# Optimization experiments

Measured on AMD Instinct MI355X. Metric: run time of the kernel, lower is better.

## Reference

```python
import jax, jax.numpy as jnp
import numpy as np

N = 100000  # nodes
E = 1600000  # directed edges

_DIMS = [("eg1", 3, 160), ("eg2", 160, 80), ("eg3", 80, 40), ("eg4", 40, 20),
         ("el1", 20, 10), ("el2", 10, 3), ("dl1", 3, 10), ("dl2", 10, 20),
         ("dg1", 20, 40), ("dg2", 40, 80), ("dg3", 80, 160), ("dg4", 160, 3)]


def _lin_init(key, ci, co):
    s = 1.0 / np.sqrt(ci)
    kw, kb = jax.random.split(key)
    w = jax.random.uniform(kw, (ci, co), jnp.float32, -s, s)
    b = jax.random.uniform(kb, (co,), jnp.float32, -s, s)
    return w, b


def setup_inputs():
    key = jax.random.key(0)
    k0, k1, k2 = jax.random.split(key, 3)
    x = jax.random.normal(k0, (N, 3), jnp.float32)
    src = jax.random.randint(k1, (E,), 0, N)
    dst = jax.random.randint(k2, (E,), 0, N)
    edge_index = jnp.stack([src, dst])  # [2, E] int32 indices
    out = {"x": x, "edge_index": edge_index}
    for i, (name, ci, co) in enumerate(_DIMS):
        w, b = _lin_init(jax.random.fold_in(key, i + 10), ci, co)
        out[name + "_w"] = w
        out[name + "_b"] = b
    return out


def _gcn(x, w, b, src, dst, norm):
    # PyG GCNConv: linear transform, then symmetric-normalized scatter-add.
    h = x @ w
    agg = jax.ops.segment_sum(h[src] * norm[:, None], dst, num_segments=N)
    return agg + b


def reference(x, edge_index, eg1_w, eg1_b, eg2_w, eg2_b, eg3_w, eg3_b, eg4_w, eg4_b,
              el1_w, el1_b, el2_w, el2_b, dl1_w, dl1_b, dl2_w, dl2_b,
              dg1_w, dg1_b, dg2_w, dg2_b, dg3_w, dg3_b, dg4_w, dg4_b):
    loops = jnp.arange(N)
    src = jnp.concatenate([edge_index[0], loops])  # add self-loops (PyG default)
    dst = jnp.concatenate([edge_index[1], loops])
    deg = jax.ops.segment_sum(jnp.ones(src.shape[0], x.dtype), dst, num_segments=N)
    dis = jnp.where(deg > 0, jax.lax.rsqrt(deg), 0.0)
    norm = dis[src] * dis[dst]  # D^-1/2 A D^-1/2 edge weights
    relu = jax.nn.relu
    h = relu(_gcn(x, eg1_w, eg1_b, src, dst, norm))
    h = relu(_gcn(h, eg2_w, eg2_b, src, dst, norm))
    h = relu(_gcn(h, eg3_w, eg3_b, src, dst, norm))
    h = relu(_gcn(h, eg4_w, eg4_b, src, dst, norm))
    h = relu(h @ el1_w + el1_b)
    h = h @ el2_w + el2_b  # latent [N, 3]
    h = relu(h @ dl1_w + dl1_b)
    h = relu(h @ dl2_w + dl2_b)
    h = relu(_gcn(h, dg1_w, dg1_b, src, dst, norm))
    h = relu(_gcn(h, dg2_w, dg2_b, src, dst, norm))
    h = relu(_gcn(h, dg3_w, dg3_b, src, dst, norm))
    h = jnp.tanh(_gcn(h, dg4_w, dg4_b, src, dst, norm))
    return h
```

## Files before the change

### kernel.cpp

```cpp
#include <hip/hip_runtime.h>
#include <hip/hip_fp16.h>
#include <math.h>

#define BS 256
static constexpr int NN = 100000;
static constexpr int EE = 1600000;
static constexpr int BUCKET_SH = 7;
static constexpr int NBUCKET = (NN + 127) >> BUCKET_SH;
static constexpr int NB_PART = 256;
static constexpr int CHUNK = EE / NB_PART;
static constexpr int NP = NBUCKET * NB_PART;
static constexpr int SCAN_ELEMS = 1024;
static constexpr int NPB = (NP + SCAN_ELEMS - 1) / SCAN_ELEMS;

static inline int cdiv(long long a, int b) { return (int)((a + b - 1) / b); }

template <int ACT>
__device__ __forceinline__ float act_f(float v) {
    if (ACT == 1) return fmaxf(v, 0.0f);
    if (ACT == 2) return tanhf(v);
    return v;
}

__device__ __forceinline__ unsigned short h16(float v) {
    return __half_as_ushort(__float2half(v));
}
__device__ __forceinline__ unsigned pack2h(float a, float b) {
    return (unsigned)h16(a) | ((unsigned)h16(b) << 16);
}
__device__ __forceinline__ float4 cvt4h(uint2 r) {
    float2 fa = __half22float2(*(const __half2*)&r.x);
    float2 fb = __half22float2(*(const __half2*)&r.y);
    return make_float4(fa.x, fa.y, fb.x, fb.y);
}

template <int OUTM>
__device__ __forceinline__ void store1(float* out, size_t idx, float v, float dn) {
    if (OUTM == 0) out[idx] = v;
    else if (OUTM == 1) out[idx] = v * dn;
    else if (OUTM == 2) ((unsigned short*)out)[idx] = h16(v * dn);
    else ((unsigned short*)out)[idx] = h16(v);
}

__global__ __launch_bounds__(256) void k_hist(const int* __restrict__ dst,
                                              int* __restrict__ part_cnt) {
    __shared__ int h[NBUCKET];
    int b = blockIdx.x;
    for (int j = threadIdx.x; j < NBUCKET; j += 256) h[j] = 0;
    __syncthreads();
    int e0 = b * CHUNK;
    for (int k = threadIdx.x; k < CHUNK; k += 256)
        atomicAdd(&h[dst[e0 + k] >> BUCKET_SH], 1);
    __syncthreads();
    for (int j = threadIdx.x; j < NBUCKET; j += 256)
        part_cnt[j * NB_PART + b] = h[j];
}

__global__ void k_scanA(const int* __restrict__ in, int* __restrict__ outp,
                        int* __restrict__ bsums) {
    __shared__ int lds[BS];
    int base = blockIdx.x * SCAN_ELEMS;
    int t = threadIdx.x;
    int v[4];
    int s = 0;
#pragma unroll
    for (int j = 0; j < 4; ++j) {
        int idx = base + t * 4 + j;
        v[j] = (idx < NP) ? in[idx] : 0;
        s += v[j];
    }
    lds[t] = s;
    __syncthreads();
    for (int off = 1; off < BS; off <<= 1) {
        int add = (t >= off) ? lds[t - off] : 0;
        __syncthreads();
        lds[t] += add;
        __syncthreads();
    }
    int run = lds[t] - s;
    if (t == BS - 1) bsums[blockIdx.x] = lds[BS - 1];
#pragma unroll
    for (int j = 0; j < 4; ++j) {
        int idx = base + t * 4 + j;
        if (idx < NP) outp[idx] = run;
        run += v[j];
    }
}

__global__ void k_scanB(int* __restrict__ bsums) {
    if (threadIdx.x == 0 && blockIdx.x == 0) {
        int acc = 0;
        for (int i = 0; i < NPB; ++i) {
            int t = bsums[i];
            bsums[i] = acc;
            acc += t;
        }
    }
}

__global__ void k_scanC(int* __restrict__ outp, const int* __restrict__ bsums,
                        int* __restrict__ bbase) {
    int i = blockIdx.x * BS + threadIdx.x;
    if (i < NP) {
        int v = outp[i] + bsums[i / SCAN_ELEMS];
        outp[i] = v;
        if ((i & (NB_PART - 1)) == 0) bbase[i / NB_PART] = v;
    }
    if (i == 0) bbase[NBUCKET] = EE;
}

__global__ __launch_bounds__(256) void k_part(const int* __restrict__ src,
                                              const int* __restrict__ dst,
                                              const int* __restrict__ scan_out,
                                              unsigned* __restrict__ epb) {
    __shared__ int cur[NBUCKET];
    int b = blockIdx.x;
    for (int j = threadIdx.x; j < NBUCKET; j += 256) cur[j] = scan_out[j * NB_PART + b];
    __syncthreads();
    int e0 = b * CHUNK;
    for (int k = threadIdx.x; k < CHUNK; k += 256) {
        int e = e0 + k;
        int d = dst[e];
        int s = src[e];
        int pos = atomicAdd(&cur[d >> BUCKET_SH], 1);
        epb[pos] = ((unsigned)(d & ((1 << BUCKET_SH) - 1)) << 17) | (unsigned)s;
    }
}

__global__ __launch_bounds__(256) void k_fine2(const int* __restrict__ bbase,
                                               const unsigned* __restrict__ epb,
                                               int* __restrict__ eidx,
                                               int* __restrict__ rowptr,
                                               float* __restrict__ dis) {
    __shared__ int hcnt[1 << BUCKET_SH];
    __shared__ int hoff[1 << BUCKET_SH];
    int b = blockIdx.x;
    int n0 = b << BUCKET_SH;
    int nloc = min(1 << BUCKET_SH, NN - n0);
    int t = threadIdx.x;
    if (t < (1 << BUCKET_SH)) hcnt[t] = 0;
    __syncthreads();
    int es = bbase[b], ee = bbase[b + 1];
    for (int k = es + t; k < ee; k += 256) atomicAdd(&hcnt[epb[k] >> 17], 1);
    __syncthreads();
    if (t < (1 << BUCKET_SH)) hoff[t] = hcnt[t];
    __syncthreads();
    for (int off = 1; off < (1 << BUCKET_SH); off <<= 1) {
        int add = (t >= off && t < (1 << BUCKET_SH)) ? hoff[t - off] : 0;
        __syncthreads();
        if (t < (1 << BUCKET_SH)) hoff[t] += add;
        __syncthreads();
    }
    if (t < nloc) {
        int excl = hoff[t] - hcnt[t];
        rowptr[n0 + t] = es + excl;
        dis[n0 + t] = rsqrtf((float)(hcnt[t] + 1));
    }
    __syncthreads();
    if (t < (1 << BUCKET_SH)) hoff[t] = es + hoff[t] - hcnt[t];
    __syncthreads();
    for (int k = es + t; k < ee; k += 256) {
        unsigned p = epb[k];
        int pos = atomicAdd(&hoff[p >> 17], 1);
        eidx[pos] = (int)(p & 0x1FFFFu);
    }
    if (b == NBUCKET - 1 && t == 0) rowptr[NN] = EE;
}

template <int C, int ACT, bool HASB>
__global__ void k_gatherh(const unsigned short* __restrict__ g, const int* __restrict__ rowptr,
                          const int* __restrict__ eidx, const float* __restrict__ dis,
                          const float* __restrict__ b, float* __restrict__ out) {
    static_assert(C % 4 == 0, "C%4");
    constexpr int V = C / 4;
    int t = blockIdx.x * BS + threadIdx.x;
    if (t >= NN * V) return;
    int n = t / V, v = t % V;
    const uint2* g2 = (const uint2*)g;
    float4 acc = cvt4h(g2[(size_t)n * V + v]);
    int rs = rowptr[n], re = rowptr[n + 1];
    int k = rs;
    for (; k + 4 <= re; k += 4) {
        int s0 = eidx[k + 0], s1 = eidx[k + 1], s2 = eidx[k + 2], s3 = eidx[k + 3];
        uint2 r0 = g2[(size_t)s0 * V + v];
        uint2 r1 = g2[(size_t)s1 * V + v];
        uint2 r2 = g2[(size_t)s2 * V + v];
        uint2 r3 = g2[(size_t)s3 * V + v];
        float4 h0 = cvt4h(r0), h1 = cvt4h(r1), h2 = cvt4h(r2), h3 = cvt4h(r3);
        acc.x += (h0.x + h1.x) + (h2.x + h3.x);
        acc.y += (h0.y + h1.y) + (h2.y + h3.y);
        acc.z += (h0.z + h1.z) + (h2.z + h3.z);
        acc.w += (h0.w + h1.w) + (h2.w + h3.w);
    }
    for (; k < re; ++k) {
        float4 hv = cvt4h(g2[(size_t)eidx[k] * V + v]);
        acc.x += hv.x; acc.y += hv.y; acc.z += hv.z; acc.w += hv.w;
    }
    float dn = dis[n];
    acc.x *= dn; acc.y *= dn; acc.z *= dn; acc.w *= dn;
    if (HASB) {
        float4 bb = ((const float4*)b)[v];
        acc.x += bb.x; acc.y += bb.y; acc.z += bb.z; acc.w += bb.w;
    }
    acc.x = act_f<ACT>(acc.x);
    acc.y = act_f<ACT>(acc.y);
    acc.z = act_f<ACT>(acc.z);
    acc.w = act_f<ACT>(acc.w);
    ((float4*)out)[(size_t)n * V + v] = acc;
}

template <int ACT, bool HASB>
__global__ void k_gather3d(const float* __restrict__ g, const int* __restrict__ rowptr,
                           const int* __restrict__ eidx, const float* __restrict__ dis,
                           const float* __restrict__ b, float* __restrict__ out) {
    int n = blockIdx.x * BS + threadIdx.x;
    if (n >= NN) return;
    const float* gp = g + (size_t)n * 3;
    float a0 = gp[0], a1 = gp[1], a2 = gp[2];
    int rs = rowptr[n], re = rowptr[n + 1];
    int k = rs;
    for (; k + 4 <= re; k += 4) {
        const float* q0 = g + (size_t)eidx[k + 0] * 3;
        const float* q1 = g + (size_t)eidx[k + 1] * 3;
        const float* q2 = g + (size_t)eidx[k + 2] * 3;
        const float* q3 = g + (size_t)eidx[k + 3] * 3;
        float b00 = q0[0], b01 = q0[1], b02 = q0[2];
        float b10 = q1[0], b11 = q1[1], b12 = q1[2];
        float b20 = q2[0], b21 = q2[1], b22 = q2[2];
        float b30 = q3[0], b31 = q3[1], b32 = q3[2];
        a0 += (b00 + b10) + (b20 + b30);
        a1 += (b01 + b11) + (b21 + b31);
        a2 += (b02 + b12) + (b22 + b32);
    }
    for (; k < re; ++k) {
        const float* gq = g + (size_t)eidx[k] * 3;
        a0 += gq[0]; a1 += gq[1]; a2 += gq[2];
    }
    float dn = dis[n];
    a0 *= dn; a1 *= dn; a2 *= dn;
    if (HASB) { a0 += b[0]; a1 += b[1]; a2 += b[2]; }
    float* op = out + (size_t)n * 3;
    op[0] = act_f<ACT>(a0);
    op[1] = act_f<ACT>(a1);
    op[2] = act_f<ACT>(a2);
}

__global__ void k_scale3(const float* __restrict__ x, const float* __restrict__ dis,
                         float* __restrict__ g) {
    int i = blockIdx.x * BS + threadIdx.x;
    if (i < NN * 3) g[i] = x[i] * dis[i / 3];
}

template <int CIN, int COUT, int TC, int TN, int TM, int BK, int ACT, bool HASB, int OUTM, bool INH>
__global__ __launch_bounds__(256) void k_mm_tiled(const float* __restrict__ x,
                                                  const float* __restrict__ w,
                                                  const float* __restrict__ b,
                                                  float* __restrict__ out,
                                                  const float* __restrict__ dis) {
    constexpr int TR = 256 / TC;
    constexpr int BM = TR * TM;
    constexpr int LDA = BM + 4;
    constexpr int CHUNKS = CIN / BK;
    constexpr int BK4 = BK / 4;
    constexpr int CIN4 = CIN / 4;
    static_assert(TC * TN == COUT, "cols");
    static_assert(CIN % BK == 0 && BK % 4 == 0, "bk");
    static_assert(TM == 4 || TM == 8, "tm");
    __shared__ float As[BK * LDA];
    __shared__ float Ws[BK * COUT];
    const int tid = threadIdx.x;
    const int tc = tid % TC, tr = tid / TC;
    const int n0 = blockIdx.x * BM;

    float acc[TM][TN];
#pragma unroll
    for (int r = 0; r < TM; ++r)
#pragma unroll
        for (int j = 0; j < TN; ++j) acc[r][j] = HASB ? b[tc * TN + j] : 0.0f;

    const float4* x4 = (const float4*)x;
    const uint2* xh = (const uint2*)x;
    const float4* w4 = (const float4*)w;

    for (int ch = 0; ch < CHUNKS; ++ch) {
        const int kb4 = ch * BK4;
        if (ch) __syncthreads();
        for (int i = tid; i < BM * BK4; i += 256) {
            int r = i / BK4, k4 = i % BK4;
            int row = n0 + r;
            float4 v = make_float4(0.f, 0.f, 0.f, 0.f);
            if (row < NN) {
                if (INH) v = cvt4h(xh[(size_t)row * CIN4 + kb4 + k4]);
                else v = x4[(size_t)row * CIN4 + kb4 + k4];
            }
            int base = (4 * k4) * LDA + r;
            As[base] = v.x;
            As[base + LDA] = v.y;
            As[base + 2 * LDA] = v.z;
            As[base + 3 * LDA] = v.w;
        }
        for (int i = tid; i < BK * COUT / 4; i += 256) {
            ((float4*)Ws)[i] = w4[(size_t)kb4 * COUT + i];
        }
        __syncthreads();
#pragma unroll 4
        for (int k = 0; k < BK; ++k) {
            float a[TM];
            *(float4*)&a[0] = *(const float4*)&As[k * LDA + tr * TM];
            if (TM == 8) *(float4*)&a[4] = *(const float4*)&As[k * LDA + tr * TM + 4];
            float wr[TN];
#pragma unroll
            for (int j = 0; j < TN; ++j) wr[j] = Ws[k * COUT + tc * TN + j];
#pragma unroll
            for (int r = 0; r < TM; ++r)
#pragma unroll
                for (int j = 0; j < TN; ++j) acc[r][j] = fmaf(a[r], wr[j], acc[r][j]);
        }
    }
#pragma unroll
    for (int r = 0; r < TM; ++r) {
        int row = n0 + tr * TM + r;
        if (row < NN) {
            float dn = (OUTM == 1 || OUTM == 2) ? dis[row] : 0.0f;
            size_t base = (size_t)row * COUT + tc * TN;
#pragma unroll
            for (int j = 0; j < TN; ++j) store1<OUTM>(out, base + j, act_f<ACT>(acc[r][j]), dn);
        }
    }
}

template <int CIN, int COUT, int ACT, bool HASB, int OUTM>
__global__ void k_mm_vec4(const float* __restrict__ x, const float* __restrict__ w,
                          const float* __restrict__ b, float* __restrict__ out,
                          const float* __restrict__ dis) {
    static_assert(CIN % 4 == 0 && COUT % 4 == 0, "align");
    constexpr int TM = 8;
    constexpr int CIN4 = CIN / 4;
    constexpr int COUT4 = COUT / 4;
    constexpr int RG = NN / TM;
    int i = blockIdx.x * BS + threadIdx.x;
    if (i >= RG * COUT4) return;
    int c4 = i % COUT4;
    int n0 = (i / COUT4) * TM;
    const float4* x4 = (const float4*)x;
    const float4* w4 = (const float4*)w;
    float4 acc[TM];
    float4 bb = HASB ? ((const float4*)b)[c4] : make_float4(0.f, 0.f, 0.f, 0.f);
#pragma unroll
    for (int r = 0; r < TM; ++r) acc[r] = bb;
    for (int k4 = 0; k4 < CIN4; ++k4) {
        float4 wv[4];
#pragma unroll
        for (int j = 0; j < 4; ++j) wv[j] = w4[(size_t)(4 * k4 + j) * COUT4 + c4];
#pragma unroll
        for (int r = 0; r < TM; ++r) {
            float4 xv = x4[(size_t)(n0 + r) * CIN4 + k4];
            acc[r].x = fmaf(xv.x, wv[0].x, fmaf(xv.y, wv[1].x, fmaf(xv.z, wv[2].x, fmaf(xv.w, wv[3].x, acc[r].x))));
            acc[r].y = fmaf(xv.x, wv[0].y, fmaf(xv.y, wv[1].y, fmaf(xv.z, wv[2].y, fmaf(xv.w, wv[3].y, acc[r].y))));
            acc[r].z = fmaf(xv.x, wv[0].z, fmaf(xv.y, wv[1].z, fmaf(xv.z, wv[2].z, fmaf(xv.w, wv[3].z, acc[r].z))));
            acc[r].w = fmaf(xv.x, wv[0].w, fmaf(xv.y, wv[1].w, fmaf(xv.z, wv[2].w, fmaf(xv.w, wv[3].w, acc[r].w))));
        }
    }
#pragma unroll
    for (int r = 0; r < TM; ++r) {
        float vx = act_f<ACT>(acc[r].x), vy = act_f<ACT>(acc[r].y);
        float vz = act_f<ACT>(acc[r].z), vw = act_f<ACT>(acc[r].w);
        size_t gi = (size_t)(n0 + r) * COUT4 + c4;
        if (OUTM == 2) {
            float dn = dis[n0 + r];
            uint2 u;
            u.x = pack2h(vx * dn, vy * dn);
            u.y = pack2h(vz * dn, vw * dn);
            ((uint2*)out)[gi] = u;
        } else if (OUTM == 1) {
            float dn = dis[n0 + r];
            ((float4*)out)[gi] = make_float4(vx * dn, vy * dn, vz * dn, vw * dn);
        } else {
            ((float4*)out)[gi] = make_float4(vx, vy, vz, vw);
        }
    }
}

template <int CIN, int COUT, int ACT, int OUTM>
__global__ void k_mm_rowbcast(const float* __restrict__ x, const float* __restrict__ w,
                              const float* __restrict__ b, float* __restrict__ out) {
    static_assert(COUT % 4 == 0, "c4");
    constexpr int COUT4 = COUT / 4;
    int i = blockIdx.x * BS + threadIdx.x;
    if (i >= NN * COUT4) return;
    int n = i / COUT4, c4 = i % COUT4;
    const float4* w4 = (const float4*)w;
    float4 acc = ((const float4*)b)[c4];
    const float* xr = x + (size_t)n * CIN;
#pragma unroll
    for (int ci = 0; ci < CIN; ++ci) {
        float xv = xr[ci];
        float4 wv = w4[ci * COUT4 + c4];
        acc.x = fmaf(xv, wv.x, acc.x);
        acc.y = fmaf(xv, wv.y, acc.y);
        acc.z = fmaf(xv, wv.z, acc.z);
        acc.w = fmaf(xv, wv.w, acc.w);
    }
    acc.x = act_f<ACT>(acc.x); acc.y = act_f<ACT>(acc.y);
    acc.z = act_f<ACT>(acc.z); acc.w = act_f<ACT>(acc.w);
    if (OUTM == 3) {
        uint2 u;
        u.x = pack2h(acc.x, acc.y);
        u.y = pack2h(acc.z, acc.w);
        ((uint2*)out)[(size_t)n * COUT4 + c4] = u;
    } else {
        ((float4*)out)[(size_t)n * COUT4 + c4] = acc;
    }
}

template <int CIN, int COUT, int ACT, bool HASB, int OUTM>
__global__ void k_mm_simple(const float* __restrict__ x, const float* __restrict__ w,
                            const float* __restrict__ b, float* __restrict__ out,
                            const float* __restrict__ dis) {
    int i = blockIdx.x * BS + threadIdx.x;
    if (i >= NN * COUT) return;
    int n = i / COUT, c = i % COUT;
    const float* xr = x + (size_t)n * CIN;
    float acc = HASB ? b[c] : 0.0f;
#pragma unroll
    for (int ci = 0; ci < CIN; ++ci) acc = fmaf(xr[ci], w[ci * COUT + c], acc);
    float dn = (OUTM == 1 || OUTM == 2) ? dis[n] : 0.0f;
    store1<OUTM>(out, (size_t)i, act_f<ACT>(acc), dn);
}

template <int CIN, int COUT, int ACT, bool HASB, int OUTM>
__global__ void k_mm_vec(const float* __restrict__ x, const float* __restrict__ w,
                         const float* __restrict__ b, float* __restrict__ out,
                         const float* __restrict__ dis) {
    static_assert(CIN % 4 == 0, "CIN%4");
    constexpr int TM = 8;
    constexpr int CIN4 = CIN / 4;
    constexpr int RG = NN / TM;
    int i = blockIdx.x * BS + threadIdx.x;
    if (i >= RG * COUT) return;
    int c = i % COUT;
    int n0 = (i / COUT) * TM;
    float acc[TM];
    float bb = HASB ? b[c] : 0.0f;
#pragma unroll
    for (int r = 0; r < TM; ++r) acc[r] = bb;
    const float4* x4 = (const float4*)x;
    for (int k = 0; k < CIN4; ++k) {
        float w0 = w[(4 * k + 0) * COUT + c];
        float w1 = w[(4 * k + 1) * COUT + c];
        float w2 = w[(4 * k + 2) * COUT + c];
        float w3 = w[(4 * k + 3) * COUT + c];
#pragma unroll
        for (int r = 0; r < TM; ++r) {
            float4 xv = x4[(size_t)(n0 + r) * CIN4 + k];
            acc[r] = fmaf(xv.x, w0, fmaf(xv.y, w1, fmaf(xv.z, w2, fmaf(xv.w, w3, acc[r]))));
        }
    }
#pragma unroll
    for (int r = 0; r < TM; ++r) {
        int row = n0 + r;
        float dn = (OUTM == 1 || OUTM == 2) ? dis[row] : 0.0f;
        store1<OUTM>(out, (size_t)row * COUT + c, act_f<ACT>(acc[r]), dn);
    }
}

extern "C" void kernel_launch(void* const* d_in, const int* in_sizes, int n_in,
                              void* d_out, int out_size, void* d_ws, size_t ws_size,
                              hipStream_t stream) {
    const float* x = (const float*)d_in[0];
    const int* ei = (const int*)d_in[1];
    const int* src = ei;
    const int* dst = ei + EE;
    const float* eg1_w = (const float*)d_in[2];  const float* eg1_b = (const float*)d_in[3];
    const float* eg2_w = (const float*)d_in[4];  const float* eg2_b = (const float*)d_in[5];
    const float* eg3_w = (const float*)d_in[6];  const float* eg3_b = (const float*)d_in[7];
    const float* eg4_w = (const float*)d_in[8];  const float* eg4_b = (const float*)d_in[9];
    const float* el1_w = (const float*)d_in[10]; const float* el1_b = (const float*)d_in[11];
    const float* el2_w = (const float*)d_in[12]; const float* el2_b = (const float*)d_in[13];
    const float* dl1_w = (const float*)d_in[14]; const float* dl1_b = (const float*)d_in[15];
    const float* dl2_w = (const float*)d_in[16]; const float* dl2_b = (const float*)d_in[17];
    const float* dg1_w = (const float*)d_in[18]; const float* dg1_b = (const float*)d_in[19];
    const float* dg2_w = (const float*)d_in[20]; const float* dg2_b = (const float*)d_in[21];
    const float* dg3_w = (const float*)d_in[22]; const float* dg3_b = (const float*)d_in[23];
    const float* dg4_w = (const float*)d_in[24]; const float* dg4_b = (const float*)d_in[25];
    float* out = (float*)d_out;

    char* ws = (char*)d_ws;
    size_t off = 0;
    auto alloc = [&](size_t bytes) {
        void* p = ws + off;
        off += (bytes + 15) & ~(size_t)15;
        return p;
    };
    int* part_cnt = (int*)alloc(sizeof(int) * NP);
    int* scan_out = (int*)alloc(sizeof(int) * NP);
    int* bsums    = (int*)alloc(sizeof(int) * NPB);
    int* bbase    = (int*)alloc(sizeof(int) * (NBUCKET + 1));
    int* rowptr   = (int*)alloc(sizeof(int) * (NN + 1));
    float* dis    = (float*)alloc(sizeof(float) * NN);
    int* eidx     = (int*)alloc(sizeof(int) * EE);
    unsigned* epb = (unsigned*)alloc(sizeof(unsigned) * EE);
    unsigned short* G = (unsigned short*)alloc(sizeof(unsigned short) * 80 * (size_t)NN);
    float* bufA = (float*)alloc(sizeof(float) * 160 * (size_t)NN);
    float* bufB = (float*)alloc(sizeof(float) * 160 * (size_t)NN);

    k_hist<<<NB_PART, 256, 0, stream>>>(dst, part_cnt);
    k_scanA<<<NPB, BS, 0, stream>>>(part_cnt, scan_out, bsums);
    k_scanB<<<1, 64, 0, stream>>>(bsums);
    k_scanC<<<cdiv(NP, BS), BS, 0, stream>>>(scan_out, bsums, bbase);
    k_part<<<NB_PART, 256, 0, stream>>>(src, dst, scan_out, epb);
    k_fine2<<<NBUCKET, 256, 0, stream>>>(bbase, epb, eidx, rowptr, dis);

    k_scale3<<<cdiv(3LL * NN, BS), BS, 0, stream>>>(x, dis, bufB);
    k_gather3d<0, false><<<cdiv(NN, BS), BS, 0, stream>>>(bufB, rowptr, eidx, dis, nullptr, bufA);
    k_mm_rowbcast<3, 160, 1, 3><<<cdiv(NN * 40LL, BS), BS, 0, stream>>>(bufA, eg1_w, eg1_b, bufB);

    k_mm_tiled<160, 80, 16, 5, 8, 32, 0, false, 2, true><<<cdiv(NN, 128), 256, 0, stream>>>(
        bufB, eg2_w, nullptr, (float*)G, dis);
    k_gatherh<80, 1, true><<<cdiv(NN * 20LL, BS), BS, 0, stream>>>(G, rowptr, eidx, dis, eg2_b, bufA);

    k_mm_tiled<80, 40, 8, 5, 4, 40, 0, false, 2, false><<<cdiv(NN, 128), 256, 0, stream>>>(
        bufA, eg3_w, nullptr, (float*)G, dis);
    k_gatherh<40, 1, true><<<cdiv(NN * 10LL, BS), BS, 0, stream>>>(G, rowptr, eidx, dis, eg3_b, bufB);

    k_mm_vec4<40, 20, 0, false, 2><<<cdiv((NN / 8) * 5LL, BS), BS, 0, stream>>>(
        bufB, eg4_w, nullptr, (float*)G, dis);
    k_gatherh<20, 1, true><<<cdiv(NN * 5LL, BS), BS, 0, stream>>>(G, rowptr, eidx, dis, eg4_b, bufA);

    k_mm_vec<20, 10, 1, true, 0><<<cdiv((NN / 8) * 10LL, BS), BS, 0, stream>>>(bufA, el1_w, el1_b, bufB, nullptr);
    k_mm_simple<10, 3, 0, true, 0><<<cdiv(3LL * NN, BS), BS, 0, stream>>>(bufB, el2_w, el2_b, bufA, nullptr);
    k_mm_simple<3, 10, 1, true, 0><<<cdiv(10LL * NN, BS), BS, 0, stream>>>(bufA, dl1_w, dl1_b, bufB, nullptr);
    k_mm_simple<10, 20, 1, true, 2><<<cdiv(20LL * NN, BS), BS, 0, stream>>>(bufB, dl2_w, dl2_b, (float*)G, dis);

    k_gatherh<20, 0, false><<<cdiv(NN * 5LL, BS), BS, 0, stream>>>(G, rowptr, eidx, dis, nullptr, bufA);
    k_mm_vec4<20, 40, 1, true, 2><<<cdiv((NN / 8) * 10LL, BS), BS, 0, stream>>>(
        bufA, dg1_w, dg1_b, (float*)G, dis);

    k_gatherh<40, 0, false><<<cdiv(NN * 10LL, BS), BS, 0, stream>>>(G, rowptr, eidx, dis, nullptr, bufB);
    k_mm_tiled<40, 80, 16, 5, 8, 40, 1, true, 2, false><<<cdiv(NN, 128), 256, 0, stream>>>(
        bufB, dg2_w, dg2_b, (float*)G, dis);

    k_gatherh<80, 0, false><<<cdiv(NN * 20LL, BS), BS, 0, stream>>>(G, rowptr, eidx, dis, nullptr, bufA);
    k_mm_tiled<80, 160, 32, 5, 8, 40, 1, true, 0, false><<<cdiv(NN, 64), 256, 0, stream>>>(
        bufA, dg3_w, dg3_b, bufB, nullptr);

    k_mm_vec<160, 3, 0, false, 1><<<cdiv((NN / 8) * 3LL, BS), BS, 0, stream>>>(bufB, dg4_w, nullptr, bufA, dis);
    k_gather3d<2, true><<<cdiv(NN, BS), BS, 0, stream>>>(bufA, rowptr, eidx, dis, dg4_b, out);
}
```

Measured before the change: 627.4 us.

## Split fp16 gather features into 20-channel chunks for cache locality

The fp16 intermediate feature buffer for the wide GCN layers (40 and 80 channels) is now stored as separate 20-channel planes, each [N,20], instead of interleaved rows. The gather kernel processes one plane per block group, so the random neighbour reads in each plane touch a 4 MB working set that fits in cache better. The matmul epilogues write into this chunked layout. In exchange, each gather pass re-reads rowptr and eidx once per chunk, and the matmul stores become scattered 16-bit writes.

```diff
diff --git a/kernel.cpp b/kernel.cpp
--- a/kernel.cpp
+++ b/kernel.cpp
@@ -167,25 +167,29 @@
     if (b == NBUCKET - 1 && t == 0) rowptr[NN] = EE;
 }
 
-template <int C, int ACT, bool HASB>
-__global__ void k_gatherh(const unsigned short* __restrict__ g, const int* __restrict__ rowptr,
-                          const int* __restrict__ eidx, const float* __restrict__ dis,
-                          const float* __restrict__ b, float* __restrict__ out) {
-    static_assert(C % 4 == 0, "C%4");
-    constexpr int V = C / 4;
-    int t = blockIdx.x * BS + threadIdx.x;
+template <int NCHUNK, int ACT, bool HASB>
+__global__ __launch_bounds__(256) void k_gatherp(const unsigned short* __restrict__ g,
+                                                 const int* __restrict__ rowptr,
+                                                 const int* __restrict__ eidx,
+                                                 const float* __restrict__ dis,
+                                                 const float* __restrict__ b,
+                                                 float* __restrict__ out) {
+    constexpr int V = 5;
+    constexpr int BPC = (NN * V + 255) / 256;
+    int chunk = blockIdx.x / BPC;
+    int t = (blockIdx.x - chunk * BPC) * 256 + threadIdx.x;
     if (t >= NN * V) return;
     int n = t / V, v = t % V;
-    const uint2* g2 = (const uint2*)g;
-    float4 acc = cvt4h(g2[(size_t)n * V + v]);
+    const uint2* gp = (const uint2*)g + (size_t)chunk * NN * V;
+    float4 acc = cvt4h(gp[(size_t)n * V + v]);
     int rs = rowptr[n], re = rowptr[n + 1];
     int k = rs;
     for (; k + 4 <= re; k += 4) {
         int s0 = eidx[k + 0], s1 = eidx[k + 1], s2 = eidx[k + 2], s3 = eidx[k + 3];
-        uint2 r0 = g2[(size_t)s0 * V + v];
-        uint2 r1 = g2[(size_t)s1 * V + v];
-        uint2 r2 = g2[(size_t)s2 * V + v];
-        uint2 r3 = g2[(size_t)s3 * V + v];
+        uint2 r0 = gp[(size_t)s0 * V + v];
+        uint2 r1 = gp[(size_t)s1 * V + v];
+        uint2 r2 = gp[(size_t)s2 * V + v];
+        uint2 r3 = gp[(size_t)s3 * V + v];
         float4 h0 = cvt4h(r0), h1 = cvt4h(r1), h2 = cvt4h(r2), h3 = cvt4h(r3);
         acc.x += (h0.x + h1.x) + (h2.x + h3.x);
         acc.y += (h0.y + h1.y) + (h2.y + h3.y);
@@ -193,20 +197,20 @@
         acc.w += (h0.w + h1.w) + (h2.w + h3.w);
     }
     for (; k < re; ++k) {
-        float4 hv = cvt4h(g2[(size_t)eidx[k] * V + v]);
+        float4 hv = cvt4h(gp[(size_t)eidx[k] * V + v]);
         acc.x += hv.x; acc.y += hv.y; acc.z += hv.z; acc.w += hv.w;
     }
     float dn = dis[n];
     acc.x *= dn; acc.y *= dn; acc.z *= dn; acc.w *= dn;
     if (HASB) {
-        float4 bb = ((const float4*)b)[v];
+        float4 bb = ((const float4*)b)[chunk * V + v];
         acc.x += bb.x; acc.y += bb.y; acc.z += bb.z; acc.w += bb.w;
     }
     acc.x = act_f<ACT>(acc.x);
     acc.y = act_f<ACT>(acc.y);
     acc.z = act_f<ACT>(acc.z);
     acc.w = act_f<ACT>(acc.w);
-    ((float4*)out)[(size_t)n * V + v] = acc;
+    ((float4*)out)[(size_t)n * (NCHUNK * V) + chunk * V + v] = acc;
 }
 
 template <int ACT, bool HASB>
@@ -321,10 +325,18 @@
     for (int r = 0; r < TM; ++r) {
         int row = n0 + tr * TM + r;
         if (row < NN) {
-            float dn = (OUTM == 1 || OUTM == 2) ? dis[row] : 0.0f;
-            size_t base = (size_t)row * COUT + tc * TN;
-#pragma unroll
-            for (int j = 0; j < TN; ++j) store1<OUTM>(out, base + j, act_f<ACT>(acc[r][j]), dn);
+            float dn = (OUTM == 1 || OUTM == 2 || OUTM == 4) ? dis[row] : 0.0f;
+            if (OUTM == 4) {
+                int c0 = tc * TN;
+                unsigned short* gout = (unsigned short*)out +
+                    (size_t)(c0 / 20) * NN * 20 + (size_t)row * 20 + (c0 % 20);
+#pragma unroll
+                for (int j = 0; j < TN; ++j) gout[j] = h16(act_f<ACT>(acc[r][j]) * dn);
+            } else {
+                size_t base = (size_t)row * COUT + tc * TN;
+#pragma unroll
+                for (int j = 0; j < TN; ++j) store1<OUTM>(out, base + j, act_f<ACT>(acc[r][j]), dn);
+            }
         }
     }
 }
@@ -365,18 +377,26 @@
     for (int r = 0; r < TM; ++r) {
         float vx = act_f<ACT>(acc[r].x), vy = act_f<ACT>(acc[r].y);
         float vz = act_f<ACT>(acc[r].z), vw = act_f<ACT>(acc[r].w);
-        size_t gi = (size_t)(n0 + r) * COUT4 + c4;
-        if (OUTM == 2) {
+        if (OUTM == 4) {
+            float dn = dis[n0 + r];
+            int c0 = c4 * 4;
+            unsigned short* gout = (unsigned short*)out +
+                (size_t)(c0 / 20) * NN * 20 + (size_t)(n0 + r) * 20 + (c0 % 20);
+            uint2 u;
+            u.x = pack2h(vx * dn, vy * dn);
+            u.y = pack2h(vz * dn, vw * dn);
+            *(uint2*)gout = u;
+        } else if (OUTM == 2) {
             float dn = dis[n0 + r];
             uint2 u;
             u.x = pack2h(vx * dn, vy * dn);
             u.y = pack2h(vz * dn, vw * dn);
-            ((uint2*)out)[gi] = u;
+            ((uint2*)out)[(size_t)(n0 + r) * COUT4 + c4] = u;
         } else if (OUTM == 1) {
             float dn = dis[n0 + r];
-            ((float4*)out)[gi] = make_float4(vx * dn, vy * dn, vz * dn, vw * dn);
+            ((float4*)out)[(size_t)(n0 + r) * COUT4 + c4] = make_float4(vx * dn, vy * dn, vz * dn, vw * dn);
         } else {
-            ((float4*)out)[gi] = make_float4(vx, vy, vz, vw);
+            ((float4*)out)[(size_t)(n0 + r) * COUT4 + c4] = make_float4(vx, vy, vz, vw);
         }
     }
 }
@@ -504,6 +524,8 @@
     float* bufA = (float*)alloc(sizeof(float) * 160 * (size_t)NN);
     float* bufB = (float*)alloc(sizeof(float) * 160 * (size_t)NN);
 
+    constexpr int BPC = (NN * 5 + 255) / 256;
+
     k_hist<<<NB_PART, 256, 0, stream>>>(dst, part_cnt);
     k_scanA<<<NPB, BS, 0, stream>>>(part_cnt, scan_out, bsums);
     k_scanB<<<1, 64, 0, stream>>>(bsums);
@@ -515,32 +537,32 @@
     k_gather3d<0, false><<<cdiv(NN, BS), BS, 0, stream>>>(bufB, rowptr, eidx, dis, nullptr, bufA);
     k_mm_rowbcast<3, 160, 1, 3><<<cdiv(NN * 40LL, BS), BS, 0, stream>>>(bufA, eg1_w, eg1_b, bufB);
 
-    k_mm_tiled<160, 80, 16, 5, 8, 32, 0, false, 2, true><<<cdiv(NN, 128), 256, 0, stream>>>(
+    k_mm_tiled<160, 80, 16, 5, 8, 32, 0, false, 4, true><<<cdiv(NN, 128), 256, 0, stream>>>(
         bufB, eg2_w, nullptr, (float*)G, dis);
-    k_gatherh<80, 1, true><<<cdiv(NN * 20LL, BS), BS, 0, stream>>>(G, rowptr, eidx, dis, eg2_b, bufA);
-
-    k_mm_tiled<80, 40, 8, 5, 4, 40, 0, false, 2, false><<<cdiv(NN, 128), 256, 0, stream>>>(
+    k_gatherp<4, 1, true><<<4 * BPC, 256, 0, stream>>>(G, rowptr, eidx, dis, eg2_b, bufA);
+
+    k_mm_tiled<80, 40, 8, 5, 4, 40, 0, false, 4, false><<<cdiv(NN, 128), 256, 0, stream>>>(
         bufA, eg3_w, nullptr, (float*)G, dis);
-    k_gatherh<40, 1, true><<<cdiv(NN * 10LL, BS), BS, 0, stream>>>(G, rowptr, eidx, dis, eg3_b, bufB);
+    k_gatherp<2, 1, true><<<2 * BPC, 256, 0, stream>>>(G, rowptr, eidx, dis, eg3_b, bufB);
 
     k_mm_vec4<40, 20, 0, false, 2><<<cdiv((NN / 8) * 5LL, BS), BS, 0, stream>>>(
         bufB, eg4_w, nullptr, (float*)G, dis);
-    k_gatherh<20, 1, true><<<cdiv(NN * 5LL, BS), BS, 0, stream>>>(G, rowptr, eidx, dis, eg4_b, bufA);
+    k_gatherp<1, 1, true><<<BPC, 256, 0, stream>>>(G, rowptr, eidx, dis, eg4_b, bufA);
 
     k_mm_vec<20, 10, 1, true, 0><<<cdiv((NN / 8) * 10LL, BS), BS, 0, stream>>>(bufA, el1_w, el1_b, bufB, nullptr);
     k_mm_simple<10, 3, 0, true, 0><<<cdiv(3LL * NN, BS), BS, 0, stream>>>(bufB, el2_w, el2_b, bufA, nullptr);
     k_mm_simple<3, 10, 1, true, 0><<<cdiv(10LL * NN, BS), BS, 0, stream>>>(bufA, dl1_w, dl1_b, bufB, nullptr);
     k_mm_simple<10, 20, 1, true, 2><<<cdiv(20LL * NN, BS), BS, 0, stream>>>(bufB, dl2_w, dl2_b, (float*)G, dis);
 
-    k_gatherh<20, 0, false><<<cdiv(NN * 5LL, BS), BS, 0, stream>>>(G, rowptr, eidx, dis, nullptr, bufA);
-    k_mm_vec4<20, 40, 1, true, 2><<<cdiv((NN / 8) * 10LL, BS), BS, 0, stream>>>(
+    k_gatherp<1, 0, false><<<BPC, 256, 0, stream>>>(G, rowptr, eidx, dis, nullptr, bufA);
+    k_mm_vec4<20, 40, 1, true, 4><<<cdiv((NN / 8) * 10LL, BS), BS, 0, stream>>>(
         bufA, dg1_w, dg1_b, (float*)G, dis);
 
-    k_gatherh<40, 0, false><<<cdiv(NN * 10LL, BS), BS, 0, stream>>>(G, rowptr, eidx, dis, nullptr, bufB);
-    k_mm_tiled<40, 80, 16, 5, 8, 40, 1, true, 2, false><<<cdiv(NN, 128), 256, 0, stream>>>(
+    k_gatherp<2, 0, false><<<2 * BPC, 256, 0, stream>>>(G, rowptr, eidx, dis, nullptr, bufB);
+    k_mm_tiled<40, 80, 16, 5, 8, 40, 1, true, 4, false><<<cdiv(NN, 128), 256, 0, stream>>>(
         bufB, dg2_w, dg2_b, (float*)G, dis);
 
-    k_gatherh<80, 0, false><<<cdiv(NN * 20LL, BS), BS, 0, stream>>>(G, rowptr, eidx, dis, nullptr, bufA);
+    k_gatherp<4, 0, false><<<4 * BPC, 256, 0, stream>>>(G, rowptr, eidx, dis, nullptr, bufA);
     k_mm_tiled<80, 160, 32, 5, 8, 40, 1, true, 0, false><<<cdiv(NN, 64), 256, 0, stream>>>(
         bufA, dg3_w, dg3_b, bufB, nullptr);
 
```

Result: slower. 674.9 us (+7.6%).
